# Performance work log

Measured on AMD Instinct MI355X. Metric: run time of the kernel, lower is better.

## Reference

```python
import jax, jax.numpy as jnp
import numpy as np

EPS = 1e-6  # annotated-transformer LayerNorm eps


def setup_inputs() -> dict:
    key = jax.random.key(0)
    ks = jax.random.split(key, 6)
    B, S, D, F, G_dom = 32, 512, 1024, 2048, 4
    x = jax.random.normal(ks[0], (B, S, D), dtype=jnp.float32)
    # disjoint partition of the batch into 4 equal domain groups (like the
    # per-domain LongTensor index lists in the torch forward)
    perm = jax.random.permutation(ks[1], B).astype(jnp.int32)
    idx = perm.reshape(G_dom, B // G_dom)  # [4, 8]
    s1 = 1.0 / np.sqrt(D)
    s2 = 1.0 / np.sqrt(F)
    W1 = jax.random.normal(ks[2], (G_dom, D, F), dtype=jnp.float32) * s1
    B1 = jnp.zeros((G_dom, F), dtype=jnp.float32)
    W2 = jax.random.normal(ks[3], (G_dom, F, D), dtype=jnp.float32) * s2
    B2 = jnp.zeros((G_dom, D), dtype=jnp.float32)
    G = jnp.ones((G_dom, D), dtype=jnp.float32)
    Bn = jnp.zeros((G_dom, D), dtype=jnp.float32)
    return {"x": x, "idx": idx, "W1": W1, "B1": B1, "W2": W2, "B2": B2,
            "G": G, "Bn": Bn}


def _layer_norm(x, g, b):
    # matches torch: a_2 * (x - mean) / (std + eps) + b_2, std unbiased (ddof=1)
    mu = jnp.mean(x, axis=-1, keepdims=True)
    sd = jnp.std(x, axis=-1, keepdims=True, ddof=1)
    return g * (x - mu) / (sd + EPS) + b


def reference(x, idx, W1, B1, W2, B2, G, Bn):
    # gather per-domain token groups: [n_dom, per_dom, S, D]
    xg = x[idx]
    # SublayerConnection (eval mode, dropout off): x + adapter(norm(x))
    h = _layer_norm(xg, G[:, None, None, :], Bn[:, None, None, :])
    h = jax.nn.relu(jnp.einsum('gbsd,gdf->gbsf', h, W1) + B1[:, None, None, :])
    a = jnp.einsum('gbsf,gfd->gbsd', h, W2) + B2[:, None, None, :]
    out_g = xg + a
    # scatter combine (index_copy): indices are a disjoint partition
    S_, D_ = x.shape[1], x.shape[2]
    out = jnp.zeros_like(x).at[idx.reshape(-1)].set(out_g.reshape(-1, S_, D_))
    return out
```

## Files before the change

kernel.cpp:

```cpp
#include <hip/hip_runtime.h>
#include <hip/hip_bf16.h>


#define S_DIM 512
#define D_DIM 1024
#define F_DIM 2048
#define MPG   4096

typedef __attribute__((ext_vector_type(8))) short  short8;
typedef __attribute__((ext_vector_type(4))) float  f32x4;

__device__ __forceinline__ void gll16(const void* g, void* l) {
  __builtin_amdgcn_global_load_lds((__attribute__((address_space(1))) void*)g,
                                   (__attribute__((address_space(3))) void*)l,
                                   16, 0, 0);
}
#define BAR()  asm volatile("s_barrier" ::: "memory")
#define VMC4() asm volatile("s_waitcnt vmcnt(4)" ::: "memory")
#define LGKM0() asm volatile("s_waitcnt lgkmcnt(0)" ::: "memory")

__global__ __launch_bounds__(256) void transpose_cast_kernel(
    const float* __restrict__ W1, const float* __restrict__ W2,
    __hip_bfloat16* __restrict__ W1t, __hip_bfloat16* __restrict__ W2t)
{
  __shared__ float tl[32][33];
  const int bid = blockIdx.x;
  const float* src; __hip_bfloat16* dst;
  int R, C, tr, tc;
  if (bid < 8192) {
    const int g = bid >> 11, t = bid & 2047;
    R = 1024; C = 2048; tr = t >> 6; tc = t & 63;
    src = W1 + (size_t)g * R * C;
    dst = W1t + (size_t)g * R * C;
  } else {
    const int b2 = bid - 8192;
    const int g = b2 >> 11, t = b2 & 2047;
    R = 2048; C = 1024; tr = t >> 5; tc = t & 31;
    src = W2 + (size_t)g * R * C;
    dst = W2t + (size_t)g * R * C;
  }
  const int tx = threadIdx.x & 31, ty = threadIdx.x >> 5;
  const int r0 = tr * 32, c0 = tc * 32;
#pragma unroll
  for (int i = 0; i < 4; ++i)
    tl[ty + 8 * i][tx] = src[(size_t)(r0 + ty + 8 * i) * C + (c0 + tx)];
  __syncthreads();
#pragma unroll
  for (int i = 0; i < 4; ++i)
    dst[(size_t)(c0 + ty + 8 * i) * R + (r0 + tx)] = __float2bfloat16(tl[tx][ty + 8 * i]);
}

__global__ __launch_bounds__(256) void ln_gather_kernel(
    const float* __restrict__ x, const int* __restrict__ idx,
    const float* __restrict__ G, const float* __restrict__ Bn,
    __hip_bfloat16* __restrict__ Xn)
{
  const int wid  = (blockIdx.x * 256 + threadIdx.x) >> 6;
  const int lane = threadIdx.x & 63;
  const int g = wid >> 12;
  const int r = wid & 4095;
  const int j = r >> 9;
  const int tok = r & 511;
  const int b = idx[g * 8 + j];

  const float* src = x + ((size_t)b * S_DIM + tok) * D_DIM + lane * 16;
  float4 vq[4];
#pragma unroll
  for (int i = 0; i < 4; ++i) vq[i] = ((const float4*)src)[i];
  const float* va = (const float*)vq;

  float s = 0.f, s2 = 0.f;
#pragma unroll
  for (int i = 0; i < 16; ++i) { s += va[i]; s2 += va[i] * va[i]; }
#pragma unroll
  for (int o = 32; o > 0; o >>= 1) { s += __shfl_xor(s, o); s2 += __shfl_xor(s2, o); }

  const float mu  = s * (1.0f / 1024.0f);
  float var = fmaxf(s2 * (1.0f / 1024.0f) - mu * mu, 0.0f) * (1024.0f / 1023.0f);
  const float rs  = 1.0f / (sqrtf(var) + 1e-6f);

  float4 gq[4], bq[4];
  const float* gp = G  + (size_t)g * D_DIM + lane * 16;
  const float* bp = Bn + (size_t)g * D_DIM + lane * 16;
#pragma unroll
  for (int i = 0; i < 4; ++i) { gq[i] = ((const float4*)gp)[i]; bq[i] = ((const float4*)bp)[i]; }
  const float* ga = (const float*)gq;
  const float* be = (const float*)bq;

  __align__(16) __hip_bfloat16 ob[16];
#pragma unroll
  for (int i = 0; i < 16; ++i)
    ob[i] = __float2bfloat16(ga[i] * (va[i] - mu) * rs + be[i]);

  __hip_bfloat16* dst = Xn + ((size_t)g * MPG + r) * D_DIM + lane * 16;
  ((uint4*)dst)[0] = *(const uint4*)&ob[0];
  ((uint4*)dst)[1] = *(const uint4*)&ob[8];
}

template <bool SECOND>
__global__ __launch_bounds__(512, 2) void gemm_kernel(
    const __hip_bfloat16* __restrict__ A,
    const __hip_bfloat16* __restrict__ Bw,
    const float* __restrict__ bias,
    const float* __restrict__ xres,
    const int* __restrict__ idx,
    __hip_bfloat16* __restrict__ obf,
    float* __restrict__ of32,
    const int N, const int K, const int NT)
{
  extern __shared__ char lds[];
  const int ntile = N >> 8;
  const int nwg = gridDim.x;
  const int bid0 = blockIdx.x;
  const int bid = (bid0 & 7) * (nwg >> 3) + (bid0 >> 3);
  const int mt = bid / ntile, nt = bid % ntile;
  const int g  = mt >> 4;
  const int tid = threadIdx.x;
  const int w = tid >> 6, lane = tid & 63;
  const int wm = w >> 2, wn = w & 3;

  const __hip_bfloat16* Ab = A + (size_t)mt * 256 * K;
  const __hip_bfloat16* Bb = Bw + ((size_t)g * N + (size_t)nt * 256) * K;

  const int sp   = (lane & 7) ^ ((lane >> 3) & 7);
  const int srow = 2 * (lane >> 3) + (sp >> 2);
  const int skof = (sp & 3) * 8;

  const int l15 = lane & 15, sl = lane >> 4;
  const int slot_phys = (((l15 & 1) << 2) + sl) ^ ((l15 >> 1) & 7);
  const int lane_c = ((l15 >> 1) << 7) + (slot_phys << 4);

  f32x4 acc[8][4] = {};

  auto stage = [&](int bufw, int mat, int kh, int tn) {
    const __hip_bfloat16* src = mat ? Bb : Ab;
    const size_t gk = (size_t)tn * 64 + kh * 32 + skof;
    char* dst = lds + bufw * 65536 + mat * 32768 + kh * 16384 + w * 2048;
    const int r0 = w * 32 + srow;
    gll16(src + (size_t)r0 * K + gk, dst);
    gll16(src + (size_t)(r0 + 16) * K + gk, dst + 1024);
  };

  stage(0, 0, 0, 0);
  stage(0, 1, 0, 0);
  stage(0, 0, 1, 0);
  stage(0, 1, 1, 0);

  short8 bfrag[4];

#define PHASE(KH, MH, SMAT, SKH, DOVM)                                          \
  {                                                                             \
    __builtin_amdgcn_sched_barrier(0);                                          \
    if (DOVM) VMC4();                                                           \
    BAR();                                                                      \
    const char* Abase = lds + bufb + (KH) * 16384 + wm * 8192 + lane_c;         \
    short8 afr[4];                                                              \
    _Pragma("unroll") for (int mm = 0; mm < 4; ++mm)                            \
      afr[mm] = *(const short8*)(Abase + ((MH) * 4 + mm) * 1024);               \
    if ((MH) == 0) {                                                            \
      const char* Bbase = lds + bufb + 32768 + (KH) * 16384 + wn * 4096 + lane_c; \
      _Pragma("unroll") for (int n = 0; n < 4; ++n)                             \
        bfrag[n] = *(const short8*)(Bbase + n * 1024);                          \
    }                                                                           \
    stage(bufn, SMAT, SKH, tn);                                                 \
    LGKM0();                                                                    \
    __builtin_amdgcn_sched_barrier(0);                                          \
    __builtin_amdgcn_s_setprio(1);                                              \
    _Pragma("unroll") for (int mm = 0; mm < 4; ++mm)                            \
      _Pragma("unroll") for (int n = 0; n < 4; ++n)                             \
        acc[(MH) * 4 + mm][n] = __builtin_amdgcn_mfma_f32_16x16x32_bf16(        \
            afr[mm], bfrag[n], acc[(MH) * 4 + mm][n], 0, 0, 0);                 \
    __builtin_amdgcn_s_setprio(0);                                              \
  }

  for (int t = 0; t < NT; ++t) {
    const int bufb = (t & 1) * 65536;
    const int bufn = (t & 1) ^ 1;
    const int tn = (t + 1 == NT) ? 0 : t + 1;
    PHASE(0, 0, 0, 0, 1)
    PHASE(0, 1, 1, 0, 0)
    PHASE(1, 0, 0, 1, 1)
    PHASE(1, 1, 1, 1, 0)
  }
#undef PHASE

  const int cc  = lane & 15;
  const int cr4 = (lane >> 4) * 4;

  float bv[4];
#pragma unroll
  for (int n = 0; n < 4; ++n)
    bv[n] = bias[(size_t)g * N + nt * 256 + wn * 64 + n * 16 + cc];

  if constexpr (!SECOND) {
#pragma unroll
    for (int m = 0; m < 8; ++m) {
      const int grow0 = mt * 256 + wm * 128 + m * 16 + cr4;
#pragma unroll
      for (int n = 0; n < 4; ++n) {
        const int gcol = nt * 256 + wn * 64 + n * 16 + cc;
#pragma unroll
        for (int i = 0; i < 4; ++i) {
          const float v = fmaxf(acc[m][n][i] + bv[n], 0.0f);
          obf[(size_t)(grow0 + i) * N + gcol] = __float2bfloat16(v);
        }
      }
    }
  } else {
    const int rbase = (mt & 15) * 256;
    const int b = idx[g * 8 + (rbase >> 9)];
    const size_t ob = (size_t)b * S_DIM * D_DIM;
#pragma unroll
    for (int m = 0; m < 8; ++m) {
      const int rloc = rbase + wm * 128 + m * 16 + cr4;
#pragma unroll
      for (int n = 0; n < 4; ++n) {
        const int gcol = nt * 256 + wn * 64 + n * 16 + cc;
#pragma unroll
        for (int i = 0; i < 4; ++i) {
          const int tok = (rloc + i) & 511;
          const size_t off = ob + (size_t)tok * D_DIM + gcol;
          of32[off] = acc[m][n][i] + bv[n] + xres[off];
        }
      }
    }
  }
}

extern "C" void kernel_launch(void* const* d_in, const int* in_sizes, int n_in,
                              void* d_out, int out_size, void* d_ws, size_t ws_size,
                              hipStream_t stream) {
  const float* x  = (const float*)d_in[0];
  const int*   idx = (const int*)d_in[1];
  const float* W1 = (const float*)d_in[2];
  const float* B1 = (const float*)d_in[3];
  const float* W2 = (const float*)d_in[4];
  const float* B2 = (const float*)d_in[5];
  const float* G  = (const float*)d_in[6];
  const float* Bn = (const float*)d_in[7];
  float* out = (float*)d_out;

  char* ws = (char*)d_ws;
  __hip_bfloat16* Xn  = (__hip_bfloat16*)(ws);
  __hip_bfloat16* W1t = (__hip_bfloat16*)(ws + 33554432);
  __hip_bfloat16* W2t = (__hip_bfloat16*)(ws + 50331648);
  __hip_bfloat16* H1  = (__hip_bfloat16*)(ws + 67108864);

  (void)hipFuncSetAttribute((const void*)gemm_kernel<false>,
                            hipFuncAttributeMaxDynamicSharedMemorySize, 131072);
  (void)hipFuncSetAttribute((const void*)gemm_kernel<true>,
                            hipFuncAttributeMaxDynamicSharedMemorySize, 131072);

  transpose_cast_kernel<<<dim3(16384), dim3(256), 0, stream>>>(W1, W2, W1t, W2t);
  ln_gather_kernel<<<dim3(4096), dim3(256), 0, stream>>>(x, idx, G, Bn, Xn);
  gemm_kernel<false><<<dim3(512), dim3(512), 131072, stream>>>(
      Xn, W1t, B1, nullptr, nullptr, H1, nullptr, F_DIM, D_DIM, 16);
  gemm_kernel<true><<<dim3(256), dim3(512), 131072, stream>>>(
      H1, W2t, B2, x, idx, nullptr, out, D_DIM, F_DIM, 32);
}
```

Measured before the change: 187.9 us.

## Software-pipeline LDS fragment reads one phase ahead of MFMA in GEMM loop

Restructures the GEMM main loop so LDS fragment reads for the next phase are issued before the current phase's MFMAs, using double-buffered register fragments instead of waiting on lgkmcnt(0) before each MFMA block. It also changes the LDS layout so the A and B halves are interleaved per k-half, precomputes the global load pointers, and adjusts the vmcnt waits. The aim is to hide LDS read latency behind matrix-core work. The cost is more registers for the extra fragments and a riskier barrier and wait ordering across buffers.

```diff
diff --git a/kernel.cpp b/kernel.cpp
--- a/kernel.cpp
+++ b/kernel.cpp
@@ -15,9 +15,10 @@
                                    (__attribute__((address_space(3))) void*)l,
                                    16, 0, 0);
 }
-#define BAR()  asm volatile("s_barrier" ::: "memory")
-#define VMC4() asm volatile("s_waitcnt vmcnt(4)" ::: "memory")
-#define LGKM0() asm volatile("s_waitcnt lgkmcnt(0)" ::: "memory")
+#define VMC2()  asm volatile("s_waitcnt vmcnt(2)" ::: "memory")
+#define VMC4()  asm volatile("s_waitcnt vmcnt(4)" ::: "memory")
+#define SB()    __builtin_amdgcn_sched_barrier(0)
+#define BAR()   __builtin_amdgcn_s_barrier()
 
 __global__ __launch_bounds__(256) void transpose_cast_kernel(
     const float* __restrict__ W1, const float* __restrict__ W2,
@@ -125,64 +126,81 @@
   const int sp   = (lane & 7) ^ ((lane >> 3) & 7);
   const int srow = 2 * (lane >> 3) + (sp >> 2);
   const int skof = (sp & 3) * 8;
+  const __hip_bfloat16* Ag0 = Ab + (size_t)(w * 32 + srow) * K + skof;
+  const __hip_bfloat16* Ag1 = Ag0 + (size_t)16 * K;
+  const __hip_bfloat16* Bg0 = Bb + (size_t)(w * 32 + srow) * K + skof;
+  const __hip_bfloat16* Bg1 = Bg0 + (size_t)16 * K;
 
   const int l15 = lane & 15, sl = lane >> 4;
   const int slot_phys = (((l15 & 1) << 2) + sl) ^ ((l15 >> 1) & 7);
   const int lane_c = ((l15 >> 1) << 7) + (slot_phys << 4);
 
   f32x4 acc[8][4] = {};
-
-  auto stage = [&](int bufw, int mat, int kh, int tn) {
-    const __hip_bfloat16* src = mat ? Bb : Ab;
-    const size_t gk = (size_t)tn * 64 + kh * 32 + skof;
-    char* dst = lds + bufw * 65536 + mat * 32768 + kh * 16384 + w * 2048;
-    const int r0 = w * 32 + srow;
-    gll16(src + (size_t)r0 * K + gk, dst);
-    gll16(src + (size_t)(r0 + 16) * K + gk, dst + 1024);
-  };
-
-  stage(0, 0, 0, 0);
-  stage(0, 1, 0, 0);
-  stage(0, 0, 1, 0);
-  stage(0, 1, 1, 0);
-
-  short8 bfrag[4];
-
-#define PHASE(KH, MH, SMAT, SKH, DOVM)                                          \
-  {                                                                             \
-    __builtin_amdgcn_sched_barrier(0);                                          \
-    if (DOVM) VMC4();                                                           \
-    BAR();                                                                      \
-    const char* Abase = lds + bufb + (KH) * 16384 + wm * 8192 + lane_c;         \
-    short8 afr[4];                                                              \
-    _Pragma("unroll") for (int mm = 0; mm < 4; ++mm)                            \
-      afr[mm] = *(const short8*)(Abase + ((MH) * 4 + mm) * 1024);               \
-    if ((MH) == 0) {                                                            \
-      const char* Bbase = lds + bufb + 32768 + (KH) * 16384 + wn * 4096 + lane_c; \
-      _Pragma("unroll") for (int n = 0; n < 4; ++n)                             \
-        bfrag[n] = *(const short8*)(Bbase + n * 1024);                          \
-    }                                                                           \
-    stage(bufn, SMAT, SKH, tn);                                                 \
-    LGKM0();                                                                    \
-    __builtin_amdgcn_sched_barrier(0);                                          \
-    __builtin_amdgcn_s_setprio(1);                                              \
-    _Pragma("unroll") for (int mm = 0; mm < 4; ++mm)                            \
-      _Pragma("unroll") for (int n = 0; n < 4; ++n)                             \
-        acc[(MH) * 4 + mm][n] = __builtin_amdgcn_mfma_f32_16x16x32_bf16(        \
-            afr[mm], bfrag[n], acc[(MH) * 4 + mm][n], 0, 0, 0);                 \
-    __builtin_amdgcn_s_setprio(0);                                              \
+  short8 frA0[4], frA1[4], frB0[4], frB1[4];
+
+#define STAGE(BUFX, MAT, KH, TN) {                                          \
+    const int koff = (TN) * 64 + (KH) * 32;                                 \
+    char* d = lds + (BUFX) + ((KH) * 2 + (MAT)) * 16384 + w * 2048;         \
+    if (MAT) { gll16(Bg0 + koff, d); gll16(Bg1 + koff, d + 1024); }         \
+    else     { gll16(Ag0 + koff, d); gll16(Ag1 + koff, d + 1024); } }
+
+#define RDA(DST, BUFX, KH, MH) {                                            \
+    const char* base_ = lds + (BUFX) + (KH) * 32768 + wm * 8192 +           \
+                        (MH) * 4096 + lane_c;                               \
+    _Pragma("unroll") for (int mm = 0; mm < 4; ++mm)                        \
+      DST[mm] = *(const short8*)(base_ + mm * 1024); }
+
+#define RDB(DST, BUFX, KH) {                                                \
+    const char* base_ = lds + (BUFX) + 16384 + (KH) * 32768 + wn * 4096 +   \
+                        lane_c;                                             \
+    _Pragma("unroll") for (int n = 0; n < 4; ++n)                           \
+      DST[n] = *(const short8*)(base_ + n * 1024); }
+
+#define MF(MH, FA, FB) {                                                    \
+    __builtin_amdgcn_s_setprio(1);                                          \
+    _Pragma("unroll") for (int mm = 0; mm < 4; ++mm)                        \
+      _Pragma("unroll") for (int n = 0; n < 4; ++n)                         \
+        acc[(MH) * 4 + mm][n] = __builtin_amdgcn_mfma_f32_16x16x32_bf16(    \
+            FA[mm], FB[n], acc[(MH) * 4 + mm][n], 0, 0, 0);                 \
+    __builtin_amdgcn_s_setprio(0); }
+
+  STAGE(0, 0, 0, 0); STAGE(0, 1, 0, 0); STAGE(0, 0, 1, 0); STAGE(0, 1, 1, 0);
+  VMC4();
+  BAR();
+  RDA(frA0, 0, 0, 0);
+  RDB(frB0, 0, 0);
+
+  for (int t = 0; t < NT; ++t) {
+    const int bufb = (t & 1) << 16;
+    const int bufx = bufb ^ 65536;
+    const int tn = (t + 1 == NT) ? 0 : t + 1;
+    SB(); BAR(); SB();
+    RDA(frA1, bufb, 0, 1);
+    STAGE(bufx, 0, 0, tn);
+    SB();
+    MF(0, frA0, frB0);
+    SB(); VMC2(); BAR(); SB();
+    RDA(frA0, bufb, 1, 0);
+    RDB(frB1, bufb, 1);
+    STAGE(bufx, 1, 0, tn);
+    SB();
+    MF(1, frA1, frB0);
+    SB(); BAR(); SB();
+    RDA(frA1, bufb, 1, 1);
+    STAGE(bufx, 0, 1, tn);
+    SB();
+    MF(0, frA0, frB1);
+    SB(); VMC2(); BAR(); SB();
+    RDA(frA0, bufx, 0, 0);
+    RDB(frB0, bufx, 0);
+    STAGE(bufx, 1, 1, tn);
+    SB();
+    MF(1, frA1, frB1);
   }
-
-  for (int t = 0; t < NT; ++t) {
-    const int bufb = (t & 1) * 65536;
-    const int bufn = (t & 1) ^ 1;
-    const int tn = (t + 1 == NT) ? 0 : t + 1;
-    PHASE(0, 0, 0, 0, 1)
-    PHASE(0, 1, 1, 0, 0)
-    PHASE(1, 0, 0, 1, 1)
-    PHASE(1, 1, 1, 1, 0)
-  }
-#undef PHASE
+#undef STAGE
+#undef RDA
+#undef RDB
+#undef MF
 
   const int cc  = lane & 15;
   const int cr4 = (lane >> 4) * 4;
```

Result: slower. 197.6 us (+5.2%).
